# Optimization experiments

Hardware: AMD Instinct MI355X
Metric: run time of the kernel (lower is better)

Reference implementation:

```python
import jax, jax.numpy as jnp
import numpy as np
from jax import lax

B = 512          # scoring batch size
NC = 10          # n_classes
N_LAB = 256      # int(B * plb), plb = 0.5 (labeled indices are the first N_LAB)
TOL = 1e-3       # gtg_t
MAX_ITER = 30    # gtg_i
INTERM = 128
CH = [64, 128, 256, 512]
SZ = [32, 16, 8, 4]
EMB = 512


def setup_inputs() -> dict:
    key = jax.random.key(0)
    ks = jax.random.split(key, 16)
    inp = {}
    for i, (c, s) in enumerate(zip(CH, SZ)):
        inp["feat%d" % i] = jax.random.normal(ks[i], (B, c, s, s), jnp.float32)
        inp["conv_w%d" % i] = jax.random.normal(ks[4 + i], (c, c, 3, 3), jnp.float32) * 0.05
        inp["conv_b%d" % i] = jnp.zeros((c,), jnp.float32)
        inp["bn_g%d" % i] = jnp.ones((c,), jnp.float32)
        inp["bn_b%d" % i] = jnp.zeros((c,), jnp.float32)
        inp["lin_w%d" % i] = jax.random.normal(ks[8 + i], (INTERM, c), jnp.float32) * 0.05
        inp["lin_b%d" % i] = jnp.zeros((INTERM,), jnp.float32)
    inp["fin_w"] = jax.random.normal(ks[12], (1, 4 * INTERM), jnp.float32) * 0.05
    inp["fin_b"] = jnp.zeros((1,), jnp.float32)
    inp["embedds"] = jax.random.normal(ks[13], (B, EMB), jnp.float32)
    inp["labels"] = jax.random.randint(ks[14], (B,), 0, NC)
    return inp


def _branch(x, cw, cb, g, b, lw, lb):
    # Conv3x3(same) -> BatchNorm (train mode, batch stats, eps=1e-5) -> ReLU -> GAP -> Linear -> ReLU
    y = lax.conv_general_dilated(x, cw, (1, 1), 'SAME',
                                 dimension_numbers=('NCHW', 'OIHW', 'NCHW')) + cb[None, :, None, None]
    m = y.mean(axis=(0, 2, 3), keepdims=True)
    v = ((y - m) ** 2).mean(axis=(0, 2, 3), keepdims=True)  # biased variance (train-mode BN)
    y = jax.nn.relu(g[None, :, None, None] * (y - m) * lax.rsqrt(v + 1e-5) + b[None, :, None, None])
    y = y.mean(axis=(2, 3))  # AvgPool2d(feature_size) == global average pool -> [B, C]
    return jax.nn.relu(y @ lw.T + lb)


def _gtg(E, labels):
    # get_A_e_d: pairwise euclidean distances clamped to [0.1, 1.0]
    sq = jnp.sum(E * E, axis=1)
    d2 = jnp.maximum(sq[:, None] + sq[None, :] - 2.0 * (E @ E.T), 0.0)
    A0 = jnp.clip(jnp.sqrt(d2), 0.1, 1.0)
    # rbf kernel: 7th nearest neighbor (ascending for 'e_d') gives per-sample sigma
    seventh = E[jnp.argsort(A0, axis=1)[:, 6]]
    sig = jnp.clip(jnp.sqrt(jnp.sum((E - seventh) ** 2, axis=1)), 0.1, 1.0)
    A = jnp.clip(jnp.exp(-(A0 ** 2) / (sig[:, None] * sig[None, :])), 0.0, 1.0)
    # threshold strategy 'mean' with AM_function == 'e_d': A = where(A > mean(A), 1, A)
    A = jnp.where(A > A.mean(), 1.0, A)
    # AM_strategy 'mixed' with 'e_d': flip only the labeled x labeled block
    A = A.at[:N_LAB, :N_LAB].set(1.0 - A[:N_LAB, :N_LAB])
    # get_X: one-hot for labeled (first N_LAB), uniform 1/NC for unlabeled
    X0 = jnp.concatenate([jax.nn.one_hot(labels[:N_LAB], NC, dtype=jnp.float32),
                          jnp.full((B - N_LAB, NC), 1.0 / NC, jnp.float32)], axis=0)
    hist0 = jnp.zeros((B, MAX_ITER), jnp.float32)

    def cond(c):
        return (c[3] > TOL) & (c[2] < MAX_ITER)

    def body(c):
        X, h, i, _ = c
        Xn = X * (A @ X)
        Xn = Xn / jnp.sum(Xn, axis=1, keepdims=True)
        ent = -jnp.sum(jnp.where(Xn > 0, Xn * jnp.log(Xn), 0.0), axis=1)
        h = lax.dynamic_update_slice(h, ent[:, None], (0, i))
        return (Xn, h, i + 1, jnp.linalg.norm(Xn - X))

    X, h, _, _ = lax.while_loop(cond, body, (X0, hist0, jnp.int32(0), jnp.float32(jnp.inf)))
    return h.mean(axis=1), X  # ent_strategy == 'mean'


def reference(feat0, feat1, feat2, feat3,
              conv_w0, conv_b0, bn_g0, bn_b0, lin_w0, lin_b0,
              conv_w1, conv_b1, bn_g1, bn_b1, lin_w1, lin_b1,
              conv_w2, conv_b2, bn_g2, bn_b2, lin_w2, lin_b2,
              conv_w3, conv_b3, bn_g3, bn_b3, lin_w3, lin_b3,
              fin_w, fin_b, embedds, labels):
    o0 = _branch(feat0, conv_w0, conv_b0, bn_g0, bn_b0, lin_w0, lin_b0)
    o1 = _branch(feat1, conv_w1, conv_b1, bn_g1, bn_b1, lin_w1, lin_b1)
    o2 = _branch(feat2, conv_w2, conv_b2, bn_g2, bn_b2, lin_w2, lin_b2)
    o3 = _branch(feat3, conv_w3, conv_b3, bn_g3, bn_b3, lin_w3, lin_b3)
    y_pred = (jnp.concatenate([o0, o1, o2, o3], axis=1) @ fin_w.T + fin_b)[:, 0]
    y_true, X = _gtg(embedds, labels)
    labeled_mask = jnp.arange(B) < N_LAB
    return (y_pred, y_true, X, labeled_mask)
```

## Files before the change

### kernel.cpp

```cpp
#include <hip/hip_runtime.h>
#include <hip/hip_bf16.h>
#include <math.h>

static constexpr int kNC = 10;
static constexpr int kNLab = 256;
static constexpr int kMaxIter = 30;

using short8 = __attribute__((ext_vector_type(8))) short;
using f32x4  = __attribute__((ext_vector_type(4))) float;

__device__ __forceinline__ unsigned short f2bf(float f) {
  unsigned int u = __float_as_uint(f);
  u += 0x7FFFu + ((u >> 16) & 1u);
  return (unsigned short)(u >> 16);
}
__device__ __forceinline__ float bf2f(unsigned short u) {
  return __uint_as_float(((unsigned int)u) << 16);
}

template <int C, int S>
__global__ __launch_bounds__(256) void xpack_kernel(const float* __restrict__ x,
                                                    unsigned short* __restrict__ xp) {
  __shared__ float t[C][S + 1];
  const int n = blockIdx.x / S, h = blockIdx.x % S;
  const float* src = x + (size_t)n * C * S * S;
  for (int e = threadIdx.x; e < C * S; e += 256) {
    int c = e / S, w = e % S;
    t[c][w] = src[((size_t)c * S + h) * S + w];
  }
  __syncthreads();
  unsigned short* dst = xp + ((size_t)(n * S + h) * S) * C;
  for (int e = threadIdx.x; e < C * S; e += 256) {
    int w = e / C, c = e % C;
    dst[(size_t)w * C + c] = f2bf(t[c][w]);
  }
}

__global__ void wpack_all(const float* __restrict__ w0, const float* __restrict__ w1,
                          const float* __restrict__ w2, const float* __restrict__ w3,
                          unsigned short* __restrict__ wpk) {
  int idx = blockIdx.x * 256 + threadIdx.x;
  if (idx >= 3133440) return;
  const float* w; int C, off;
  if (idx < 36864)        { w = w0; C = 64;  off = 0; }
  else if (idx < 184320)  { w = w1; C = 128; off = 36864; }
  else if (idx < 774144)  { w = w2; C = 256; off = 184320; }
  else                    { w = w3; C = 512; off = 774144; }
  int e = idx - off;
  int CO16T = C / 16, CIK = C / 32;
  int e8 = e & 7, l = (e >> 3) & 63;
  int rest = e >> 9;
  int co16 = rest % CO16T;
  int rest2 = rest / CO16T;
  int cik = rest2 % CIK, tap = rest2 / CIK;
  int co = co16 * 16 + (l & 15);
  int ci = cik * 32 + (l >> 4) * 8 + e8;
  wpk[idx] = f2bf(w[((size_t)co * C + ci) * 9 + tap]);
}

template <int C, int S, int NI, int NR, int WV, int BF, int MODE>
__global__ __launch_bounds__(WV * 64)
void conv_mfma(const unsigned short* __restrict__ xp, const unsigned short* __restrict__ wpk,
               const float* __restrict__ bias, unsigned short* __restrict__ y,
               float* __restrict__ psum, float* __restrict__ psq, int npart, int partBase,
               const float* __restrict__ scale, const float* __restrict__ shift,
               float* __restrict__ pp, int pxGlobalBase) {
  constexpr int SS = S * S;
  constexpr int PXB = NI * NR * S;
  constexpr int TPB = WV * 64;
  constexpr int HR = NR + 2, HC = S + 2;
  constexpr int CIK = C / 32, CO16T = C / 16;
  constexpr int UNITS = NI * HR * HC * 4;
  constexpr int NU = (UNITS + TPB - 1) / TPB;
  static_assert(WV * BF * 16 == PXB, "wave px mismatch");
  static_assert(MODE != 2 || BF == 4, "MODE2 assumes 64px/wave");
  __shared__ __align__(16) char xs[NI * HR * HC * 80];

  const int tid = threadIdx.x;
  const int wv = tid >> 6, l = tid & 63, l15 = l & 15, l4 = l >> 4;
  const int coblk = blockIdx.y;
  const int co_base = coblk * 64;
  const int pxb = blockIdx.x * PXB;
  const int n_t = pxb / SS;
  const int r0 = (pxb % SS) / S;

  int pxoff[BF];
#pragma unroll
  for (int bf = 0; bf < BF; ++bf) {
    int pxloc = wv * (BF * 16) + bf * 16 + l15;
    int ii = pxloc / (NR * S);
    int rr = (pxloc % (NR * S)) / S;
    int cc = pxloc % S;
    pxoff[bf] = ((ii * HR + rr) * HC + cc) * 80 + l4 * 16;
  }

  f32x4 acc[4][BF];
#pragma unroll
  for (int a = 0; a < 4; ++a)
#pragma unroll
    for (int b = 0; b < BF; ++b) acc[a][b] = (f32x4){0.f, 0.f, 0.f, 0.f};

  uint4 vreg[NU];
  auto loadU = [&](int cik) {
#pragma unroll
    for (int k = 0; k < NU; ++k) {
      int u = tid + k * TPB;
      uint4 v = {0u, 0u, 0u, 0u};
      if (u < UNITS) {
        int k16 = u & 3;
        int t = u >> 2;
        int hc = t % HC;
        int t2 = t / HC;
        int hr = t2 % HR;
        int ii = t2 / HR;
        int row = r0 + hr - 1, col = hc - 1;
        if (row >= 0 && row < S && col >= 0 && col < S)
          v = *(const uint4*)(xp + ((size_t)((n_t + ii) * S + row) * S + col) * C + cik * 32 + k16 * 8);
      }
      vreg[k] = v;
    }
  };

  loadU(0);
  for (int cik = 0; cik < CIK; ++cik) {
    __syncthreads();
#pragma unroll
    for (int k = 0; k < NU; ++k) {
      int u = tid + k * TPB;
      if (u < UNITS) *(uint4*)(xs + (u >> 2) * 80 + (u & 3) * 16) = vreg[k];
    }
    __syncthreads();
    if (cik + 1 < CIK) loadU(cik + 1);
#pragma unroll
    for (int tap = 0; tap < 9; ++tap) {
      const int tapoff = ((tap / 3) * HC + (tap % 3)) * 80;
      short8 wf[4], xf[BF];
#pragma unroll
      for (int af = 0; af < 4; ++af)
        wf[af] = *(const short8*)(wpk + ((size_t)((tap * CIK + cik) * CO16T + coblk * 4 + af) * 64 + l) * 8);
#pragma unroll
      for (int bf = 0; bf < BF; ++bf)
        xf[bf] = *(const short8*)(xs + pxoff[bf] + tapoff);
#pragma unroll
      for (int af = 0; af < 4; ++af)
#pragma unroll
        for (int bf = 0; bf < BF; ++bf)
          acc[af][bf] = __builtin_amdgcn_mfma_f32_16x16x32_bf16(wf[af], xf[bf], acc[af][bf], 0, 0, 0);
    }
  }

#pragma unroll
  for (int af = 0; af < 4; ++af) {
    const int co0 = co_base + af * 16 + l4 * 4;
    float4 bv = *(const float4*)(bias + co0);
    float s[4] = {0.f, 0.f, 0.f, 0.f}, q[4] = {0.f, 0.f, 0.f, 0.f};
    float4 sc4, sh4;
    if (MODE == 2) {
      sc4 = *(const float4*)(scale + co0);
      sh4 = *(const float4*)(shift + co0);
    }
#pragma unroll
    for (int bf = 0; bf < BF; ++bf) {
      float o[4];
#pragma unroll
      for (int r = 0; r < 4; ++r) o[r] = acc[af][bf][r] + ((const float*)&bv)[r];
      if (MODE == 0) {
        ushort4 pk;
        pk.x = f2bf(o[0]); pk.y = f2bf(o[1]); pk.z = f2bf(o[2]); pk.w = f2bf(o[3]);
        size_t px = (size_t)(pxb + wv * (BF * 16) + bf * 16 + l15);
        *(ushort4*)(y + px * C + co0) = pk;
      }
      if (MODE == 2) {
#pragma unroll
        for (int r = 0; r < 4; ++r)
          s[r] += fmaxf(fmaf(((const float*)&sc4)[r], o[r], ((const float*)&sh4)[r]), 0.f);
      } else {
#pragma unroll
        for (int r = 0; r < 4; ++r) { s[r] += o[r]; q[r] += o[r] * o[r]; }
      }
    }
#pragma unroll
    for (int m = 1; m < 16; m <<= 1) {
#pragma unroll
      for (int r = 0; r < 4; ++r) {
        s[r] += __shfl_xor(s[r], m);
        if (MODE != 2) q[r] += __shfl_xor(q[r], m);
      }
    }
    if (l15 == 0) {
      if (MODE == 2) {
        int n = (pxGlobalBase + pxb) / SS;
        int qw = ((pxGlobalBase + pxb) % SS) / 64 + wv;
#pragma unroll
        for (int r = 0; r < 4; ++r)
          pp[((size_t)(n * C + co0 + r)) * 16 + qw] = s[r];
      } else {
        int part = partBase + blockIdx.x * WV + wv;
#pragma unroll
        for (int r = 0; r < 4; ++r) {
          psum[(size_t)(co0 + r) * npart + part] = s[r];
          psq[(size_t)(co0 + r) * npart + part] = q[r];
        }
      }
    }
  }
}

__global__ __launch_bounds__(256)
void stats2_kernel(const float* __restrict__ psum, const float* __restrict__ psq,
                   const float* __restrict__ g, const float* __restrict__ bb,
                   float* __restrict__ scale, float* __restrict__ shift,
                   int npart, float invN) {
  int c = blockIdx.x;
  __shared__ float rs[256], rq[256];
  float s = 0.f, q = 0.f;
  for (int p = threadIdx.x; p < npart; p += 256) {
    s += psum[(size_t)c * npart + p];
    q += psq[(size_t)c * npart + p];
  }
  rs[threadIdx.x] = s; rq[threadIdx.x] = q;
  __syncthreads();
  for (int st = 128; st; st >>= 1) {
    if (threadIdx.x < st) { rs[threadIdx.x] += rs[threadIdx.x + st]; rq[threadIdx.x] += rq[threadIdx.x + st]; }
    __syncthreads();
  }
  if (threadIdx.x == 0) {
    float m = rs[0] * invN;
    float v = rq[0] * invN - m * m;
    float sc = g[c] / sqrtf(v + 1e-5f);
    scale[c] = sc;
    shift[c] = bb[c] - m * sc;
  }
}

template <int C, int S>
__global__ __launch_bounds__(256)
void pool_lin(const unsigned short* __restrict__ y, const float* __restrict__ scale,
              const float* __restrict__ shift, const float* __restrict__ lw,
              const float* __restrict__ lb, float* __restrict__ oc, int brOff) {
  constexpr int SS = S * S;
  int n = blockIdx.x;
  const unsigned short* yr = y + (size_t)n * SS * C;
  __shared__ float pl[C];
  if (C >= 256) {
    for (int co = threadIdx.x; co < C; co += 256) {
      float sc = scale[co], sh = shift[co], s = 0.f;
      for (int p = 0; p < SS; ++p) s += fmaxf(fmaf(sc, bf2f(yr[(size_t)p * C + co]), sh), 0.f);
      pl[co] = s * (1.f / SS);
    }
  } else {
    constexpr int G = 256 / C;
    int co = threadIdx.x % C;
    int sl = threadIdx.x / C;
    float sc = scale[co], sh = shift[co], s = 0.f;
    for (int p = sl; p < SS; p += G) s += fmaxf(fmaf(sc, bf2f(yr[(size_t)p * C + co]), sh), 0.f);
    __shared__ float red[256];
    red[threadIdx.x] = s;
    __syncthreads();
    if (threadIdx.x < C) {
      float t = 0.f;
      for (int gg = 0; gg < G; ++gg) t += red[gg * C + co];
      pl[co] = t * (1.f / SS);
    }
  }
  __syncthreads();
  if (threadIdx.x < 128) {
    int j = threadIdx.x;
    const float* wr = lw + (size_t)j * C;
    float s = 0.f;
    for (int t = 0; t < C; ++t) s = fmaf(pl[t], wr[t], s);
    s += lb[j];
    oc[n * 512 + brOff + j] = fmaxf(s, 0.f);
  }
}

__global__ void poolfin_kernel(const float* __restrict__ pp, float* __restrict__ pooled) {
  int i = blockIdx.x * 256 + threadIdx.x;
  if (i >= 512 * 64) return;
  float s = 0.f;
  for (int qn = 0; qn < 16; ++qn) s += pp[(size_t)i * 16 + qn];
  pooled[i] = s * (1.f / 1024.f);
}

__global__ void lin_kernel(const float* __restrict__ pooled, const float* __restrict__ lw,
                           const float* __restrict__ lb, float* __restrict__ oc,
                           int C, int brOff) {
  int idx = blockIdx.x * 256 + threadIdx.x;
  if (idx >= 512 * 128) return;
  int j = idx & 127, n = idx >> 7;
  const float4* pr = (const float4*)(pooled + (size_t)n * C);
  const float4* wr = (const float4*)(lw + (size_t)j * C);
  float s = 0.f;
  for (int t = 0; t < C / 4; ++t) {
    float4 a = pr[t], b = wr[t];
    s += a.x * b.x + a.y * b.y + a.z * b.z + a.w * b.w;
  }
  s += lb[j];
  oc[n * 512 + brOff + j] = fmaxf(s, 0.f);
}

__global__ void ypred_kernel(const float* __restrict__ oc, const float* __restrict__ fw,
                             const float* __restrict__ fb, float* __restrict__ out) {
  int wv = threadIdx.x >> 6, l = threadIdx.x & 63;
  int n = blockIdx.x * 4 + wv;
  float s = 0.f;
  for (int k = l; k < 512; k += 64) s += oc[n * 512 + k] * fw[k];
#pragma unroll
  for (int m = 32; m; m >>= 1) s += __shfl_down(s, m);
  if (l == 0) out[n] = s + fb[0];
}

__global__ void sqnorm_kernel(const float* __restrict__ E, float* __restrict__ sq) {
  int wv = threadIdx.x >> 6, l = threadIdx.x & 63;
  int n = blockIdx.x * 4 + wv;
  const float* row = E + (size_t)n * 512;
  float s = 0.f;
  for (int k = l; k < 512; k += 64) { float v = row[k]; s += v * v; }
#pragma unroll
  for (int m = 32; m; m >>= 1) s += __shfl_down(s, m);
  if (l == 0) sq[n] = s;
}

__global__ __launch_bounds__(256) void a0_kernel(const float* __restrict__ E,
                                                 const float* __restrict__ sq,
                                                 float* __restrict__ A0) {
  int bi = blockIdx.x / 32, bj = blockIdx.x % 32;
  int ti = threadIdx.x % 16, tj = threadIdx.x / 16;
  __shared__ float Ei[16][68], Ej[16][68];
  float acc = 0.f;
  for (int k0 = 0; k0 < 512; k0 += 64) {
    for (int e = threadIdx.x; e < 1024; e += 256) {
      int rr = e >> 6, cc = e & 63;
      Ei[rr][cc] = E[(size_t)(bi * 16 + rr) * 512 + k0 + cc];
      Ej[rr][cc] = E[(size_t)(bj * 16 + rr) * 512 + k0 + cc];
    }
    __syncthreads();
#pragma unroll 16
    for (int kk = 0; kk < 64; ++kk) acc = fmaf(Ei[tj][kk], Ej[ti][kk], acc);
    __syncthreads();
  }
  int i = bi * 16 + tj, j = bj * 16 + ti;
  float d2 = fmaxf(sq[i] + sq[j] - 2.f * acc, 0.f);
  A0[(size_t)i * 512 + j] = fminf(fmaxf(sqrtf(d2), 0.1f), 1.0f);
}

__global__ void seventh_kernel(const float* __restrict__ A0, int* __restrict__ idx7) {
  int i = blockIdx.x * 256 + threadIdx.x;
  if (i >= 512) return;
  float v[7]; int ix[7];
#pragma unroll
  for (int t = 0; t < 7; ++t) { v[t] = 3.4e38f; ix[t] = 0; }
  const float* row = A0 + (size_t)i * 512;
  for (int j = 0; j < 512; ++j) {
    float a = row[j];
    if (a < v[6]) {
      int pos = 6;
      while (pos > 0 && a < v[pos - 1]) { v[pos] = v[pos - 1]; ix[pos] = ix[pos - 1]; --pos; }
      v[pos] = a; ix[pos] = j;
    }
  }
  idx7[i] = ix[6];
}

__global__ void sig_kernel(const float* __restrict__ E, const int* __restrict__ idx7,
                           float* __restrict__ sig) {
  int wv = threadIdx.x >> 6, l = threadIdx.x & 63;
  int n = blockIdx.x * 4 + wv;
  const float* r1 = E + (size_t)n * 512;
  const float* r2 = E + (size_t)idx7[n] * 512;
  float s = 0.f;
  for (int k = l; k < 512; k += 64) { float d = r1[k] - r2[k]; s += d * d; }
#pragma unroll
  for (int m = 32; m; m >>= 1) s += __shfl_down(s, m);
  if (l == 0) sig[n] = fminf(fmaxf(sqrtf(s), 0.1f), 1.0f);
}

__global__ void aexp_kernel(const float* __restrict__ A0, const float* __restrict__ sig,
                            float* __restrict__ A, float* __restrict__ part) {
  int t = blockIdx.x * 256 + threadIdx.x;
  int base = t * 4;
  int i = base >> 9, j0 = base & 511;
  float si = sig[i];
  float4 a = *(const float4*)(A0 + base);
  float4 o;
  o.x = fminf(fmaxf(expf(-a.x * a.x / (si * sig[j0 + 0])), 0.f), 1.f);
  o.y = fminf(fmaxf(expf(-a.y * a.y / (si * sig[j0 + 1])), 0.f), 1.f);
  o.z = fminf(fmaxf(expf(-a.z * a.z / (si * sig[j0 + 2])), 0.f), 1.f);
  o.w = fminf(fmaxf(expf(-a.w * a.w / (si * sig[j0 + 3])), 0.f), 1.f);
  *(float4*)(A + base) = o;
  float lsum = o.x + o.y + o.z + o.w;
#pragma unroll
  for (int m = 32; m; m >>= 1) lsum += __shfl_down(lsum, m);
  __shared__ float sred[4];
  if ((threadIdx.x & 63) == 0) sred[threadIdx.x >> 6] = lsum;
  __syncthreads();
  if (threadIdx.x == 0) part[blockIdx.x] = sred[0] + sred[1] + sred[2] + sred[3];
}

__global__ void meanred_kernel(const float* __restrict__ part, float* __restrict__ meanA) {
  if (threadIdx.x == 0 && blockIdx.x == 0) {
    float s = 0.f;
    for (int p = 0; p < 256; ++p) s += part[p];
    meanA[0] = s * (1.0f / 262144.0f);
  }
}

__global__ void thresh_kernel(float* __restrict__ A, const float* __restrict__ meanA) {
  int t = blockIdx.x * 256 + threadIdx.x;
  int base = t * 4;
  int i = base >> 9, j0 = base & 511;
  float m = meanA[0];
  float4 v = *(const float4*)(A + base);
  v.x = v.x > m ? 1.f : v.x;
  v.y = v.y > m ? 1.f : v.y;
  v.z = v.z > m ? 1.f : v.z;
  v.w = v.w > m ? 1.f : v.w;
  if (i < kNLab && j0 < kNLab) {
    v.x = 1.f - v.x; v.y = 1.f - v.y; v.z = 1.f - v.z; v.w = 1.f - v.w;
  }
  *(float4*)(A + base) = v;
}

__global__ void apack_kernel(const float* __restrict__ A, float* __restrict__ Apk) {
  int t = blockIdx.x * 256 + threadIdx.x;
  if (t >= 16384) return;
  int q = t >> 10, tid = t & 1023;
  int w = tid >> 6, l = tid & 63;
  int i = w * 16 + (l & 15), g = l >> 4;
  float4 v = *(const float4*)(A + (size_t)(256 + i) * 512 + 256 + g * 64 + q * 4);
  *(float4*)(Apk + (size_t)t * 4) = v;
}

__global__ __launch_bounds__(1024) __attribute__((amdgpu_waves_per_eu(4, 4)))
void gtg3(const float* __restrict__ Apk, const float* __restrict__ A,
          const int* __restrict__ labels, float* __restrict__ out) {
  const int tid = threadIdx.x;
  const int w = tid >> 6, l = tid & 63;
  const int r = l & 15, g = l >> 4;
  const int i = w * 16 + r;
  __shared__ __align__(16) float Xs[2][3088];
  __shared__ float dredw[2][16];
  __shared__ int labs[256];

  if (tid < 256) labs[tid] = labels[tid];
  for (int e = tid; e < 3088; e += 1024) {
    int o = e % 772;
    Xs[0][e] = (o < 768 && (o % 12) < 10) ? 0.1f : 0.f;
  }
  __syncthreads();

  float areg[64];
#pragma unroll
  for (int q = 0; q < 16; ++q) {
    float4 v = *(const float4*)(Apk + ((size_t)q * 1024 + tid) * 4);
    areg[q * 4 + 0] = v.x; areg[q * 4 + 1] = v.y;
    areg[q * 4 + 2] = v.z; areg[q * 4 + 3] = v.w;
  }
#pragma unroll
  for (int k = 0; k < 64; ++k) asm volatile("" : "+v"(areg[k]));

  const float* Arl = A + (size_t)(256 + i) * 512 + g * 64;
  float lp[10];
#pragma unroll
  for (int c = 0; c < 10; ++c) lp[c] = 0.f;
#pragma unroll
  for (int q = 0; q < 16; ++q) {
    float4 v = *(const float4*)(Arl + q * 4);
    float av[4] = {v.x, v.y, v.z, v.w};
#pragma unroll
    for (int k = 0; k < 4; ++k) {
      int lab = labs[g * 64 + q * 4 + k];
#pragma unroll
      for (int c = 0; c < 10; ++c) lp[c] += (lab == c) ? av[k] : 0.f;
    }
  }
#pragma unroll
  for (int c = 0; c < 10; ++c) asm volatile("" : "+v"(lp[c]));

  const int irow = (i >> 6) * 772 + (i & 63) * 12;

  float entsum = 0.f;
  float nrm2 = 1e30f;
  int cur = 0;
  for (int it = 0; it < kMaxIter; ++it) {
    if (it > 0 && sqrtf(nrm2) <= 0.001f) break;
    const float* Xc = &Xs[cur][0];
    float ax[10];
#pragma unroll
    for (int c = 0; c < 10; ++c) ax[c] = lp[c];
#pragma unroll
    for (int jj = 0; jj < 64; ++jj) {
      const float* xr = Xc + g * 772 + jj * 12;
      float4 x0 = *(const float4*)(xr);
      float4 x1 = *(const float4*)(xr + 4);
      float2 x2 = *(const float2*)(xr + 8);
      float a = areg[jj];
      ax[0] = fmaf(a, x0.x, ax[0]); ax[1] = fmaf(a, x0.y, ax[1]);
      ax[2] = fmaf(a, x0.z, ax[2]); ax[3] = fmaf(a, x0.w, ax[3]);
      ax[4] = fmaf(a, x1.x, ax[4]); ax[5] = fmaf(a, x1.y, ax[5]);
      ax[6] = fmaf(a, x1.z, ax[6]); ax[7] = fmaf(a, x1.w, ax[7]);
      ax[8] = fmaf(a, x2.x, ax[8]); ax[9] = fmaf(a, x2.y, ax[9]);
    }
#pragma unroll
    for (int c = 0; c < 10; ++c) {
      ax[c] += __shfl_xor(ax[c], 16);
      ax[c] += __shfl_xor(ax[c], 32);
    }
    float dp = 0.f;
    if (g == 0) {
      const float* xo = Xc + irow;
      float* xn_p = &Xs[cur ^ 1][irow];
      float xn[10], ssum = 0.f;
#pragma unroll
      for (int c = 0; c < 10; ++c) { xn[c] = xo[c] * ax[c]; ssum += xn[c]; }
      float ent = 0.f;
#pragma unroll
      for (int c = 0; c < 10; ++c) {
        float xv = xn[c] / ssum;
        if (xv > 0.f) ent -= xv * logf(xv);
        float d = xv - xo[c];
        dp += d * d;
        xn_p[c] = xv;
      }
      entsum += ent;
    }
#pragma unroll
    for (int m = 1; m < 64; m <<= 1) dp += __shfl_xor(dp, m);
    if (l == 0) dredw[it & 1][w] = dp;
    __syncthreads();
    float s = 0.f;
#pragma unroll
    for (int q = 0; q < 16; ++q) s += dredw[it & 1][q];
    nrm2 = s;
    cur ^= 1;
  }

  if (g == 0) out[512 + 256 + i] = entsum * (1.0f / 30.0f);
  for (int e = tid; e < 256; e += 1024) {
    out[512 + e] = 0.f;
    out[6144 + e] = 1.f;
    out[6144 + 256 + e] = 0.f;
  }
  for (int e = tid; e < 2560; e += 1024) {
    int rr = e / 10, c = e % 10;
    out[1024 + e] = (labs[rr] == c) ? 1.f : 0.f;
    out[1024 + 2560 + e] = Xs[cur][(rr >> 6) * 772 + (rr & 63) * 12 + c];
  }
}

extern "C" void kernel_launch(void* const* d_in, const int* in_sizes, int n_in,
                              void* d_out, int out_size, void* d_ws, size_t ws_size,
                              hipStream_t stream) {
  (void)in_sizes; (void)n_in; (void)out_size;

  const float* feat[4]; const float* cw[4]; const float* cbp[4];
  const float* bg[4]; const float* bbp[4]; const float* lw[4]; const float* lbp[4];
  for (int b = 0; b < 4; ++b) {
    int base = b * 7;
    feat[b] = (const float*)d_in[base + 0];
    cw[b]  = (const float*)d_in[base + 1];
    cbp[b] = (const float*)d_in[base + 2];
    bg[b]  = (const float*)d_in[base + 3];
    bbp[b] = (const float*)d_in[base + 4];
    lw[b]  = (const float*)d_in[base + 5];
    lbp[b] = (const float*)d_in[base + 6];
  }
  const float* finw = (const float*)d_in[28];
  const float* finb = (const float*)d_in[29];
  const float* emb  = (const float*)d_in[30];
  const int* labels = (const int*)d_in[31];
  float* out = (float*)d_out;

  float* wsf = (float*)d_ws;
  unsigned short* xpad = (unsigned short*)wsf;
  unsigned short* yP   = (unsigned short*)(wsf + 4194304);
  unsigned short* wpk  = (unsigned short*)(wsf + 12582912);
  size_t off = 14149632;
  float* psum = wsf + off; off += 524288;
  float* psq  = wsf + off; off += 524288;
  float* pp   = wsf + off; off += 524288;
  float* scale = wsf + off; off += 512;
  float* shift = wsf + off; off += 512;
  float* pooled = wsf + off; off += 491520;
  float* oc = wsf + off; off += 262144;
  float* sq = wsf + off; off += 512;
  float* A0 = wsf + off; off += 262144;
  float* Am = wsf + off; off += 262144;
  float* sig = wsf + off; off += 512;
  int* idx7 = (int*)(wsf + off); off += 512;
  float* meanPart = wsf + off; off += 256;
  float* meanA = wsf + off; off += 4;
  float* Apk = wsf + off; off += 65536;
  size_t yb0_off = off;
  unsigned short* yB0 = (unsigned short*)(wsf + yb0_off);
  const bool bigB0 = ws_size >= (yb0_off + 16777216) * sizeof(float);

  unsigned short* wpkB[4] = {wpk, wpk + 36864, wpk + 184320, wpk + 774144};

  wpack_all<<<(3133440 + 255) / 256, 256, 0, stream>>>(cw[0], cw[1], cw[2], cw[3], wpk);

  for (int c = 0; c < 2; ++c) {
    xpack_kernel<128, 16><<<256 * 16, 256, 0, stream>>>(feat[1] + (size_t)c * 8388608, xpad);
    conv_mfma<128, 16, 1, 8, 4, 2, 0><<<dim3(512, 2), 256, 0, stream>>>(
        xpad, wpkB[1], cbp[1], yP + (size_t)c * 8388608, psum, psq, 4096, c * 2048,
        nullptr, nullptr, nullptr, 0);
  }
  stats2_kernel<<<128, 256, 0, stream>>>(psum, psq, bg[1], bbp[1], scale, shift, 4096, 1.f / 131072.f);
  pool_lin<128, 16><<<512, 256, 0, stream>>>(yP, scale, shift, lw[1], lbp[1], oc, 128);

  xpack_kernel<256, 8><<<512 * 8, 256, 0, stream>>>(feat[2], xpad);
  conv_mfma<256, 8, 2, 8, 4, 2, 0><<<dim3(256, 4), 256, 0, stream>>>(
      xpad, wpkB[2], cbp[2], yP, psum, psq, 1024, 0, nullptr, nullptr, nullptr, 0);
  stats2_kernel<<<256, 256, 0, stream>>>(psum, psq, bg[2], bbp[2], scale, shift, 1024, 1.f / 32768.f);
  pool_lin<256, 8><<<512, 256, 0, stream>>>(yP, scale, shift, lw[2], lbp[2], oc, 256);

  xpack_kernel<512, 4><<<512 * 4, 256, 0, stream>>>(feat[3], xpad);
  conv_mfma<512, 4, 8, 4, 4, 2, 0><<<dim3(64, 8), 256, 0, stream>>>(
      xpad, wpkB[3], cbp[3], yP, psum, psq, 256, 0, nullptr, nullptr, nullptr, 0);
  stats2_kernel<<<512, 256, 0, stream>>>(psum, psq, bg[3], bbp[3], scale, shift, 256, 1.f / 8192.f);
  pool_lin<512, 4><<<512, 256, 0, stream>>>(yP, scale, shift, lw[3], lbp[3], oc, 384);

  if (bigB0) {
    for (int c = 0; c < 4; ++c) {
      xpack_kernel<64, 32><<<128 * 32, 256, 0, stream>>>(feat[0] + (size_t)c * 8388608, xpad);
      conv_mfma<64, 32, 1, 8, 4, 4, 0><<<dim3(512, 1), 256, 0, stream>>>(
          xpad, wpkB[0], cbp[0], yB0 + (size_t)c * 8388608, psum, psq, 8192, c * 2048,
          nullptr, nullptr, nullptr, 0);
    }
    stats2_kernel<<<64, 256, 0, stream>>>(psum, psq, bg[0], bbp[0], scale, shift, 8192, 1.f / 524288.f);
    pool_lin<64, 32><<<512, 256, 0, stream>>>(yB0, scale, shift, lw[0], lbp[0], oc, 0);
  } else {
    for (int c = 0; c < 4; ++c) {
      xpack_kernel<64, 32><<<128 * 32, 256, 0, stream>>>(feat[0] + (size_t)c * 8388608, xpad);
      conv_mfma<64, 32, 1, 8, 4, 4, 1><<<dim3(512, 1), 256, 0, stream>>>(
          xpad, wpkB[0], cbp[0], nullptr, psum, psq, 8192, c * 2048, nullptr, nullptr, nullptr, 0);
    }
    stats2_kernel<<<64, 256, 0, stream>>>(psum, psq, bg[0], bbp[0], scale, shift, 8192, 1.f / 524288.f);
    for (int c = 0; c < 4; ++c) {
      xpack_kernel<64, 32><<<128 * 32, 256, 0, stream>>>(feat[0] + (size_t)c * 8388608, xpad);
      conv_mfma<64, 32, 1, 8, 4, 4, 2><<<dim3(512, 1), 256, 0, stream>>>(
          xpad, wpkB[0], cbp[0], nullptr, nullptr, nullptr, 0, 0, scale, shift, pp, c * 131072);
    }
    poolfin_kernel<<<128, 256, 0, stream>>>(pp, pooled);
    lin_kernel<<<256, 256, 0, stream>>>(pooled, lw[0], lbp[0], oc, 64, 0);
  }

  ypred_kernel<<<128, 256, 0, stream>>>(oc, finw, finb, out);
  sqnorm_kernel<<<128, 256, 0, stream>>>(emb, sq);
  a0_kernel<<<1024, 256, 0, stream>>>(emb, sq, A0);
  seventh_kernel<<<2, 256, 0, stream>>>(A0, idx7);
  sig_kernel<<<128, 256, 0, stream>>>(emb, idx7, sig);
  aexp_kernel<<<256, 256, 0, stream>>>(A0, sig, Am, meanPart);
  meanred_kernel<<<1, 64, 0, stream>>>(meanPart, meanA);
  thresh_kernel<<<256, 256, 0, stream>>>(Am, meanA);

  apack_kernel<<<64, 256, 0, stream>>>(Am, Apk);
  gtg3<<<1, 1024, 0, stream>>>(Apk, Am, labels, out);
}
```

Measured before the change: 990.3 us.

## Retile GTG iteration so each lane handles four rows across sixteen column groups

The single-block GTG replicator kernel is remapped so each 16-lane group covers 4 unlabeled rows, and each lane covers 16 columns instead of 64. This lets each X row loaded from LDS feed 4 rows of FMAs, cutting LDS reads per iteration, at the cost of a wider 4-step shuffle reduction over 40 accumulators. The labeled-part product is now built from a packed copy and stored in shared memory rather than held in registers, and the X buffer padding is changed to match the new layout. The pack kernel now also writes the labeled columns.

```diff
diff --git a/kernel.cpp b/kernel.cpp
--- a/kernel.cpp
+++ b/kernel.cpp
@@ -423,29 +423,37 @@
 
 __global__ void apack_kernel(const float* __restrict__ A, float* __restrict__ Apk) {
   int t = blockIdx.x * 256 + threadIdx.x;
-  if (t >= 16384) return;
+  if (t >= 32768) return;
   int q = t >> 10, tid = t & 1023;
   int w = tid >> 6, l = tid & 63;
-  int i = w * 16 + (l & 15), g = l >> 4;
-  float4 v = *(const float4*)(A + (size_t)(256 + i) * 512 + 256 + g * 64 + q * 4);
+  int i4 = w * 4 + (l >> 4), g = l & 15;
+  int qq = q & 15;
+  int rr = qq >> 2, jq = qq & 3;
+  int row = i4 * 4 + rr;
+  int col = g * 16 + jq * 4 + ((q < 16) ? 256 : 0);
+  float4 v = *(const float4*)(A + (size_t)(256 + row) * 512 + col);
   *(float4*)(Apk + (size_t)t * 4) = v;
 }
 
 __global__ __launch_bounds__(1024) __attribute__((amdgpu_waves_per_eu(4, 4)))
-void gtg3(const float* __restrict__ Apk, const float* __restrict__ A,
-          const int* __restrict__ labels, float* __restrict__ out) {
+void gtg4(const float* __restrict__ Apk, const int* __restrict__ labels,
+          float* __restrict__ out) {
   const int tid = threadIdx.x;
   const int w = tid >> 6, l = tid & 63;
-  const int r = l & 15, g = l >> 4;
-  const int i = w * 16 + r;
-  __shared__ __align__(16) float Xs[2][3088];
+  const int p = l >> 4;
+  const int g = l & 15;
+  const int i4 = w * 4 + p;
+
+  __shared__ __align__(16) float Xs[2][3136];
+  __shared__ float Lp[256][10];
   __shared__ float dredw[2][16];
   __shared__ int labs[256];
 
-  if (tid < 256) labs[tid] = labels[tid];
-  for (int e = tid; e < 3088; e += 1024) {
-    int o = e % 772;
-    Xs[0][e] = (o < 768 && (o % 12) < 10) ? 0.1f : 0.f;
+  if (tid < 256) {
+    labs[tid] = labels[tid];
+    int o = tid * 12 + (tid >> 4) * 4;
+#pragma unroll
+    for (int c = 0; c < 10; ++c) Xs[0][o + c] = 0.1f;
   }
   __syncthreads();
 
@@ -453,76 +461,105 @@
 #pragma unroll
   for (int q = 0; q < 16; ++q) {
     float4 v = *(const float4*)(Apk + ((size_t)q * 1024 + tid) * 4);
-    areg[q * 4 + 0] = v.x; areg[q * 4 + 1] = v.y;
-    areg[q * 4 + 2] = v.z; areg[q * 4 + 3] = v.w;
+    int base = (q >> 2) * 16 + (q & 3) * 4;
+    areg[base + 0] = v.x; areg[base + 1] = v.y;
+    areg[base + 2] = v.z; areg[base + 3] = v.w;
   }
 #pragma unroll
   for (int k = 0; k < 64; ++k) asm volatile("" : "+v"(areg[k]));
 
-  const float* Arl = A + (size_t)(256 + i) * 512 + g * 64;
-  float lp[10];
-#pragma unroll
-  for (int c = 0; c < 10; ++c) lp[c] = 0.f;
-#pragma unroll
-  for (int q = 0; q < 16; ++q) {
-    float4 v = *(const float4*)(Arl + q * 4);
-    float av[4] = {v.x, v.y, v.z, v.w};
-#pragma unroll
-    for (int k = 0; k < 4; ++k) {
-      int lab = labs[g * 64 + q * 4 + k];
-#pragma unroll
-      for (int c = 0; c < 10; ++c) lp[c] += (lab == c) ? av[k] : 0.f;
-    }
-  }
-#pragma unroll
-  for (int c = 0; c < 10; ++c) asm volatile("" : "+v"(lp[c]));
-
-  const int irow = (i >> 6) * 772 + (i & 63) * 12;
-
-  float entsum = 0.f;
+  {
+    float lpv[40];
+#pragma unroll
+    for (int e = 0; e < 40; ++e) lpv[e] = 0.f;
+#pragma unroll
+    for (int q = 0; q < 16; ++q) {
+      float4 v = *(const float4*)(Apk + ((size_t)(16 + q) * 1024 + tid) * 4);
+      int rr = q >> 2, jj0 = (q & 3) * 4;
+      float av[4] = {v.x, v.y, v.z, v.w};
+#pragma unroll
+      for (int k = 0; k < 4; ++k) {
+        int lab = labs[g * 16 + jj0 + k];
+#pragma unroll
+        for (int c = 0; c < 10; ++c) lpv[rr * 10 + c] += (lab == c) ? av[k] : 0.f;
+      }
+    }
+#pragma unroll
+    for (int m = 1; m < 16; m <<= 1)
+#pragma unroll
+      for (int e = 0; e < 40; ++e) lpv[e] += __shfl_xor(lpv[e], m);
+    if (g == 0) {
+#pragma unroll
+      for (int rr = 0; rr < 4; ++rr)
+#pragma unroll
+        for (int c = 0; c < 10; ++c) Lp[i4 * 4 + rr][c] = lpv[rr * 10 + c];
+    }
+  }
+  __syncthreads();
+
+  const int gbase = g * 196;
+
+  float entsum[4] = {0.f, 0.f, 0.f, 0.f};
   float nrm2 = 1e30f;
   int cur = 0;
   for (int it = 0; it < kMaxIter; ++it) {
     if (it > 0 && sqrtf(nrm2) <= 0.001f) break;
     const float* Xc = &Xs[cur][0];
-    float ax[10];
-#pragma unroll
-    for (int c = 0; c < 10; ++c) ax[c] = lp[c];
-#pragma unroll
-    for (int jj = 0; jj < 64; ++jj) {
-      const float* xr = Xc + g * 772 + jj * 12;
+    float ax[40];
+#pragma unroll
+    for (int e = 0; e < 40; ++e) ax[e] = 0.f;
+#pragma unroll
+    for (int jj = 0; jj < 16; ++jj) {
+      const float* xr = Xc + gbase + jj * 12;
       float4 x0 = *(const float4*)(xr);
       float4 x1 = *(const float4*)(xr + 4);
       float2 x2 = *(const float2*)(xr + 8);
-      float a = areg[jj];
-      ax[0] = fmaf(a, x0.x, ax[0]); ax[1] = fmaf(a, x0.y, ax[1]);
-      ax[2] = fmaf(a, x0.z, ax[2]); ax[3] = fmaf(a, x0.w, ax[3]);
-      ax[4] = fmaf(a, x1.x, ax[4]); ax[5] = fmaf(a, x1.y, ax[5]);
-      ax[6] = fmaf(a, x1.z, ax[6]); ax[7] = fmaf(a, x1.w, ax[7]);
-      ax[8] = fmaf(a, x2.x, ax[8]); ax[9] = fmaf(a, x2.y, ax[9]);
-    }
-#pragma unroll
-    for (int c = 0; c < 10; ++c) {
-      ax[c] += __shfl_xor(ax[c], 16);
-      ax[c] += __shfl_xor(ax[c], 32);
-    }
+#pragma unroll
+      for (int rr = 0; rr < 4; ++rr) {
+        float a = areg[rr * 16 + jj];
+        ax[rr * 10 + 0] = fmaf(a, x0.x, ax[rr * 10 + 0]);
+        ax[rr * 10 + 1] = fmaf(a, x0.y, ax[rr * 10 + 1]);
+        ax[rr * 10 + 2] = fmaf(a, x0.z, ax[rr * 10 + 2]);
+        ax[rr * 10 + 3] = fmaf(a, x0.w, ax[rr * 10 + 3]);
+        ax[rr * 10 + 4] = fmaf(a, x1.x, ax[rr * 10 + 4]);
+        ax[rr * 10 + 5] = fmaf(a, x1.y, ax[rr * 10 + 5]);
+        ax[rr * 10 + 6] = fmaf(a, x1.z, ax[rr * 10 + 6]);
+        ax[rr * 10 + 7] = fmaf(a, x1.w, ax[rr * 10 + 7]);
+        ax[rr * 10 + 8] = fmaf(a, x2.x, ax[rr * 10 + 8]);
+        ax[rr * 10 + 9] = fmaf(a, x2.y, ax[rr * 10 + 9]);
+      }
+    }
+#pragma unroll
+    for (int m = 1; m < 16; m <<= 1)
+#pragma unroll
+      for (int e = 0; e < 40; ++e) ax[e] += __shfl_xor(ax[e], m);
+
     float dp = 0.f;
     if (g == 0) {
-      const float* xo = Xc + irow;
-      float* xn_p = &Xs[cur ^ 1][irow];
-      float xn[10], ssum = 0.f;
-#pragma unroll
-      for (int c = 0; c < 10; ++c) { xn[c] = xo[c] * ax[c]; ssum += xn[c]; }
-      float ent = 0.f;
-#pragma unroll
-      for (int c = 0; c < 10; ++c) {
-        float xv = xn[c] / ssum;
-        if (xv > 0.f) ent -= xv * logf(xv);
-        float d = xv - xo[c];
-        dp += d * d;
-        xn_p[c] = xv;
+#pragma unroll
+      for (int rr = 0; rr < 4; ++rr) {
+        int row = i4 * 4 + rr;
+        int off = row * 12 + (row >> 4) * 4;
+        const float* xo = Xc + off;
+        float* xn_p = &Xs[cur ^ 1][off];
+        float xn[10], ssum = 0.f;
+#pragma unroll
+        for (int c = 0; c < 10; ++c) {
+          float s = ax[rr * 10 + c] + Lp[row][c];
+          xn[c] = xo[c] * s;
+          ssum += xn[c];
+        }
+        float ent = 0.f;
+#pragma unroll
+        for (int c = 0; c < 10; ++c) {
+          float xv = xn[c] / ssum;
+          if (xv > 0.f) ent -= xv * logf(xv);
+          float d = xv - xo[c];
+          dp += d * d;
+          xn_p[c] = xv;
+        }
+        entsum[rr] += ent;
       }
-      entsum += ent;
     }
 #pragma unroll
     for (int m = 1; m < 64; m <<= 1) dp += __shfl_xor(dp, m);
@@ -535,7 +572,11 @@
     cur ^= 1;
   }
 
-  if (g == 0) out[512 + 256 + i] = entsum * (1.0f / 30.0f);
+  if (g == 0) {
+#pragma unroll
+    for (int rr = 0; rr < 4; ++rr)
+      out[512 + 256 + i4 * 4 + rr] = entsum[rr] * (1.0f / 30.0f);
+  }
   for (int e = tid; e < 256; e += 1024) {
     out[512 + e] = 0.f;
     out[6144 + e] = 1.f;
@@ -544,7 +585,7 @@
   for (int e = tid; e < 2560; e += 1024) {
     int rr = e / 10, c = e % 10;
     out[1024 + e] = (labs[rr] == c) ? 1.f : 0.f;
-    out[1024 + 2560 + e] = Xs[cur][(rr >> 6) * 772 + (rr & 63) * 12 + c];
+    out[1024 + 2560 + e] = Xs[cur][rr * 12 + (rr >> 4) * 4 + c];
   }
 }
 
@@ -590,7 +631,7 @@
   int* idx7 = (int*)(wsf + off); off += 512;
   float* meanPart = wsf + off; off += 256;
   float* meanA = wsf + off; off += 4;
-  float* Apk = wsf + off; off += 65536;
+  float* Apk = wsf + off; off += 131072;
   size_t yb0_off = off;
   unsigned short* yB0 = (unsigned short*)(wsf + yb0_off);
   const bool bigB0 = ws_size >= (yb0_off + 16777216) * sizeof(float);
@@ -654,6 +695,6 @@
   meanred_kernel<<<1, 64, 0, stream>>>(meanPart, meanA);
   thresh_kernel<<<256, 256, 0, stream>>>(Am, meanA);
 
-  apack_kernel<<<64, 256, 0, stream>>>(Am, Apk);
-  gtg3<<<1, 1024, 0, stream>>>(Apk, Am, labels, out);
-}
+  apack_kernel<<<128, 256, 0, stream>>>(Am, Apk);
+  gtg4<<<1, 1024, 0, stream>>>(Apk, labels, out);
+}
```

New measurement: 1.405 ms. 41.8% more time.

## Split GTG iteration kernel into multiple launched segments with global state carry

Applied to the files above, without the earlier changes.

The single-block GTG kernel is split into four launches of up to eight iterations each, saving X, per-row entropy sums and the residual norm to workspace between segments. The register-pinning asm barriers and the waves-per-EU attribute are dropped. The mean reduction kernel now uses a parallel shared-memory tree. The split adds launch overhead and reloads of the affinity matrix on each segment.

```diff
diff --git a/kernel.cpp b/kernel.cpp
--- a/kernel.cpp
+++ b/kernel.cpp
@@ -398,11 +398,14 @@
 }
 
 __global__ void meanred_kernel(const float* __restrict__ part, float* __restrict__ meanA) {
-  if (threadIdx.x == 0 && blockIdx.x == 0) {
-    float s = 0.f;
-    for (int p = 0; p < 256; ++p) s += part[p];
-    meanA[0] = s * (1.0f / 262144.0f);
-  }
+  __shared__ float red[256];
+  red[threadIdx.x] = part[threadIdx.x];
+  __syncthreads();
+  for (int st = 128; st; st >>= 1) {
+    if (threadIdx.x < st) red[threadIdx.x] += red[threadIdx.x + st];
+    __syncthreads();
+  }
+  if (threadIdx.x == 0) meanA[0] = red[0] * (1.0f / 262144.0f);
 }
 
 __global__ void thresh_kernel(float* __restrict__ A, const float* __restrict__ meanA) {
@@ -431,9 +434,11 @@
   *(float4*)(Apk + (size_t)t * 4) = v;
 }
 
-__global__ __launch_bounds__(1024) __attribute__((amdgpu_waves_per_eu(4, 4)))
-void gtg3(const float* __restrict__ Apk, const float* __restrict__ A,
-          const int* __restrict__ labels, float* __restrict__ out) {
+__global__ __launch_bounds__(1024)
+void gtg3_seg(const float* __restrict__ Apk, const float* __restrict__ A,
+              const int* __restrict__ labels, float* __restrict__ out,
+              float* __restrict__ Xg, float* __restrict__ entsumG,
+              float* __restrict__ nrm2G, int itBase, int nIt, int last) {
   const int tid = threadIdx.x;
   const int w = tid >> 6, l = tid & 63;
   const int r = l & 15, g = l >> 4;
@@ -443,9 +448,16 @@
   __shared__ int labs[256];
 
   if (tid < 256) labs[tid] = labels[tid];
-  for (int e = tid; e < 3088; e += 1024) {
-    int o = e % 772;
-    Xs[0][e] = (o < 768 && (o % 12) < 10) ? 0.1f : 0.f;
+  if (itBase == 0) {
+    for (int e = tid; e < 3088; e += 1024) {
+      int o = e % 772;
+      Xs[0][e] = (o < 768 && (o % 12) < 10) ? 0.1f : 0.f;
+    }
+  } else {
+    for (int e = tid; e < 2560; e += 1024) {
+      int row = e / 10, c = e % 10;
+      Xs[0][(row >> 6) * 772 + (row & 63) * 12 + c] = Xg[e];
+    }
   }
   __syncthreads();
 
@@ -456,8 +468,6 @@
     areg[q * 4 + 0] = v.x; areg[q * 4 + 1] = v.y;
     areg[q * 4 + 2] = v.z; areg[q * 4 + 3] = v.w;
   }
-#pragma unroll
-  for (int k = 0; k < 64; ++k) asm volatile("" : "+v"(areg[k]));
 
   const float* Arl = A + (size_t)(256 + i) * 512 + g * 64;
   float lp[10];
@@ -474,15 +484,14 @@
       for (int c = 0; c < 10; ++c) lp[c] += (lab == c) ? av[k] : 0.f;
     }
   }
-#pragma unroll
-  for (int c = 0; c < 10; ++c) asm volatile("" : "+v"(lp[c]));
 
   const int irow = (i >> 6) * 772 + (i & 63) * 12;
 
-  float entsum = 0.f;
-  float nrm2 = 1e30f;
+  float entsum = (itBase == 0) ? 0.f : ((g == 0) ? entsumG[i] : 0.f);
+  float nrm2 = (itBase == 0) ? 1e30f : nrm2G[0];
   int cur = 0;
-  for (int it = 0; it < kMaxIter; ++it) {
+  for (int itl = 0; itl < nIt; ++itl) {
+    int it = itBase + itl;
     if (it > 0 && sqrtf(nrm2) <= 0.001f) break;
     const float* Xc = &Xs[cur][0];
     float ax[10];
@@ -526,25 +535,34 @@
     }
 #pragma unroll
     for (int m = 1; m < 64; m <<= 1) dp += __shfl_xor(dp, m);
-    if (l == 0) dredw[it & 1][w] = dp;
+    if (l == 0) dredw[itl & 1][w] = dp;
     __syncthreads();
     float s = 0.f;
 #pragma unroll
-    for (int q = 0; q < 16; ++q) s += dredw[it & 1][q];
+    for (int q = 0; q < 16; ++q) s += dredw[itl & 1][q];
     nrm2 = s;
     cur ^= 1;
   }
 
-  if (g == 0) out[512 + 256 + i] = entsum * (1.0f / 30.0f);
-  for (int e = tid; e < 256; e += 1024) {
-    out[512 + e] = 0.f;
-    out[6144 + e] = 1.f;
-    out[6144 + 256 + e] = 0.f;
-  }
   for (int e = tid; e < 2560; e += 1024) {
-    int rr = e / 10, c = e % 10;
-    out[1024 + e] = (labs[rr] == c) ? 1.f : 0.f;
-    out[1024 + 2560 + e] = Xs[cur][(rr >> 6) * 772 + (rr & 63) * 12 + c];
+    int row = e / 10, c = e % 10;
+    Xg[e] = Xs[cur][(row >> 6) * 772 + (row & 63) * 12 + c];
+  }
+  if (g == 0) entsumG[i] = entsum;
+  if (tid == 0) nrm2G[0] = nrm2;
+
+  if (last) {
+    if (g == 0) out[512 + 256 + i] = entsum * (1.0f / 30.0f);
+    for (int e = tid; e < 256; e += 1024) {
+      out[512 + e] = 0.f;
+      out[6144 + e] = 1.f;
+      out[6144 + 256 + e] = 0.f;
+    }
+    for (int e = tid; e < 2560; e += 1024) {
+      int rr = e / 10, c = e % 10;
+      out[1024 + e] = (labs[rr] == c) ? 1.f : 0.f;
+      out[1024 + 2560 + e] = Xs[cur][(rr >> 6) * 772 + (rr & 63) * 12 + c];
+    }
   }
 }
 
@@ -591,6 +609,9 @@
   float* meanPart = wsf + off; off += 256;
   float* meanA = wsf + off; off += 4;
   float* Apk = wsf + off; off += 65536;
+  float* XgG = wsf + off; off += 2560;
+  float* entG = wsf + off; off += 256;
+  float* nrmG = wsf + off; off += 4;
   size_t yb0_off = off;
   unsigned short* yB0 = (unsigned short*)(wsf + yb0_off);
   const bool bigB0 = ws_size >= (yb0_off + 16777216) * sizeof(float);
@@ -651,9 +672,12 @@
   seventh_kernel<<<2, 256, 0, stream>>>(A0, idx7);
   sig_kernel<<<128, 256, 0, stream>>>(emb, idx7, sig);
   aexp_kernel<<<256, 256, 0, stream>>>(A0, sig, Am, meanPart);
-  meanred_kernel<<<1, 64, 0, stream>>>(meanPart, meanA);
+  meanred_kernel<<<1, 256, 0, stream>>>(meanPart, meanA);
   thresh_kernel<<<256, 256, 0, stream>>>(Am, meanA);
 
   apack_kernel<<<64, 256, 0, stream>>>(Am, Apk);
-  gtg3<<<1, 1024, 0, stream>>>(Apk, Am, labels, out);
-}
+  gtg3_seg<<<1, 1024, 0, stream>>>(Apk, Am, labels, out, XgG, entG, nrmG, 0, 8, 0);
+  gtg3_seg<<<1, 1024, 0, stream>>>(Apk, Am, labels, out, XgG, entG, nrmG, 8, 8, 0);
+  gtg3_seg<<<1, 1024, 0, stream>>>(Apk, Am, labels, out, XgG, entG, nrmG, 16, 8, 0);
+  gtg3_seg<<<1, 1024, 0, stream>>>(Apk, Am, labels, out, XgG, entG, nrmG, 24, 6, 1);
+}
```

Result: slower. 1.082 ms (+9.3%).
